# Optimization experiments

Measured on AMD Instinct MI355X. Metric: run time of the kernel, lower is better.

Reference implementation:

```python
import jax, jax.numpy as jnp
import numpy as np

B, S, H, NH = 16, 384, 1024, 16
HD = H // NH  # head_dim = 64

def setup_inputs() -> dict:
    key = jax.random.key(0)
    k1, k2, k3 = jax.random.split(key, 3)
    activation = jax.random.normal(k1, (B, S, H), dtype=jnp.float32)
    attention_mask = jnp.zeros((B, 1, 1, S), dtype=jnp.float32)  # additive mask
    qkv_weight = jax.random.normal(k2, (H, 3 * H), dtype=jnp.float32) * 0.02
    qkv_bias = jax.random.normal(k3, (3 * H,), dtype=jnp.float32) * 0.02
    return {"activation": activation, "attention_mask": attention_mask,
            "qkv_weight": qkv_weight, "qkv_bias": qkv_bias}

def reference(activation, attention_mask, qkv_weight, qkv_bias):
    # op1: fused QKV projection
    qkv = activation @ qkv_weight + qkv_bias            # [B,S,3H]
    q, k, v = jnp.split(qkv, 3, axis=-1)                # each [B,S,H]
    # op2-6: split heads -> [B,NH,S,HD]
    def heads(x):
        return x.reshape(B, S, NH, HD).transpose(0, 2, 1, 3)
    q, k, v = heads(q), heads(k), heads(v)
    # op7: QK^T
    scores = jnp.einsum('bhqd,bhkd->bhqk', q, k)        # [B,NH,S,S]
    # op8: scale + mask + softmax (scale applied to scores, then additive mask)
    scale = 1.0 / np.sqrt(HD).astype(np.float32)
    probs = jax.nn.softmax(scores * scale + attention_mask, axis=-1)
    # op9: weighted V
    out = jnp.einsum('bhqk,bhkd->bhqd', probs, v)       # [B,NH,S,HD]
    # op10: concat heads
    return out.transpose(0, 2, 1, 3).reshape(B, S, H)
```

## Files before the change

### kernel.cpp

```cpp
#include <hip/hip_runtime.h>
#include <hip/hip_bf16.h>

#define BB 16
#define SS 384
#define HH 1024
#define NH 16
#define HD 64
#define MM (BB*SS)
#define KK HH
#define N3 (3*HH)

typedef float f32x4 __attribute__((ext_vector_type(4)));
typedef __bf16 bf16x8 __attribute__((ext_vector_type(8)));
typedef unsigned short us8 __attribute__((ext_vector_type(8)));
typedef unsigned short us4 __attribute__((ext_vector_type(4)));

__device__ __forceinline__ void gload_lds16(const void* g, void* l) {
    __builtin_amdgcn_global_load_lds(
        (const __attribute__((address_space(1))) void*)g,
        (__attribute__((address_space(3))) void*)l, 16, 0, 0);
}

__device__ __forceinline__ unsigned short f2b(float f) {
    __bf16 h = (__bf16)f;
    return __builtin_bit_cast(unsigned short, h);
}

__global__ __launch_bounds__(256) void cvt_x(const float4* __restrict__ in,
                                             us4* __restrict__ out, int n4) {
    int i = blockIdx.x * 256 + threadIdx.x;
    if (i < n4) {
        float4 v = in[i];
        us4 o;
        o.x = f2b(v.x); o.y = f2b(v.y); o.z = f2b(v.z); o.w = f2b(v.w);
        out[i] = o;
    }
}

__global__ __launch_bounds__(256) void cvt_w(const float* __restrict__ Wf,
                                             __bf16* __restrict__ WT) {
    __shared__ float tile[32][33];
    const int n0 = blockIdx.x * 32, k0 = blockIdx.y * 32;
    const int t = threadIdx.x;
    const int tj = t & 31, ti = t >> 5;
#pragma unroll
    for (int p = 0; p < 4; ++p) {
        int i = p * 8 + ti;
        tile[i][tj] = Wf[(size_t)(k0 + i) * N3 + n0 + tj];
    }
    __syncthreads();
#pragma unroll
    for (int p = 0; p < 4; ++p) {
        int jj = p * 8 + ti;
        WT[(size_t)(n0 + jj) * KK + k0 + tj] = (__bf16)tile[tj][jj];
    }
}

__global__ __launch_bounds__(256) void qkv_gemm(const __bf16* __restrict__ Xb,
                                                const __bf16* __restrict__ WT,
                                                const float* __restrict__ bias,
                                                __bf16* __restrict__ QKb,
                                                __bf16* __restrict__ VTg) {
    __shared__ __bf16 As[128 * 32];
    __shared__ __bf16 Bs[128 * 32];
    const int t = threadIdx.x;
    const int w = t >> 6, lane = t & 63;
    const int wr = w >> 1, wc = w & 1;
    const int l15 = lane & 15, lg = lane >> 4;
    const int m0 = blockIdx.y * 128, n0 = blockIdx.x * 128;

    f32x4 acc[4][4] = {};

    for (int k0 = 0; k0 < KK; k0 += 32) {
#pragma unroll
        for (int i = 0; i < 2; ++i) {
            int slab = w * 2 + i;
            int row = slab * 16 + (lane >> 2);
            int ck = lane & 3;
            gload_lds16(Xb + (size_t)(m0 + row) * KK + k0 + ck * 8, &As[slab * 512]);
            gload_lds16(WT + (size_t)(n0 + row) * KK + k0 + ck * 8, &Bs[slab * 512]);
        }
        __syncthreads();

        bf16x8 a[4];
#pragma unroll
        for (int i = 0; i < 4; ++i) {
            int row = wr * 64 + i * 16 + l15;
            a[i] = *(const bf16x8*)&As[row * 32 + lg * 8];
        }
#pragma unroll
        for (int j = 0; j < 4; ++j) {
            int row = wc * 64 + j * 16 + l15;
            bf16x8 bv = *(const bf16x8*)&Bs[row * 32 + lg * 8];
#pragma unroll
            for (int i = 0; i < 4; ++i)
                acc[i][j] = __builtin_amdgcn_mfma_f32_16x16x32_bf16(a[i], bv, acc[i][j], 0, 0, 0);
        }
        __syncthreads();
    }

#pragma unroll
    for (int j = 0; j < 4; ++j) {
        int c = n0 + wc * 64 + j * 16 + l15;
        float bv = bias[c];
#pragma unroll
        for (int i = 0; i < 4; ++i) {
#pragma unroll
            for (int r = 0; r < 4; ++r) {
                int rr = m0 + wr * 64 + i * 16 + lg * 4 + r;
                float v = acc[i][j][r] + bv;
                if (c < 2048) {
                    QKb[(size_t)rr * 2048 + c] = (__bf16)v;
                } else {
                    int d = c & 63;
                    int hh = (c - 2048) >> 6;
                    int bb = rr / SS;
                    int s = rr - bb * SS;
                    VTg[((size_t)(bb * NH + hh) * HD + d) * SS + s] = (__bf16)v;
                }
            }
        }
    }
}

#define KLOFF 0
#define VTOFF 49152
#define PLOFF 98304
#define QLOFF 147456
#define MKOFF 155648
#define SMEMSZ 157184

__global__ __launch_bounds__(256) void attn(const __bf16* __restrict__ QKb,
                                            const __bf16* __restrict__ VTg,
                                            const float* __restrict__ maskg,
                                            float* __restrict__ out) {
    extern __shared__ char smem[];
    const int head = blockIdx.x;
    const int b = head >> 4, h = head & 15;
    const int t = threadIdx.x;
    const int w = t >> 6, lane = t & 63;
    const int l15 = lane & 15, lg = lane >> 4;

    for (int it = 0; it < 12; ++it) {
        int slot = it * 256 + t;
        int row = slot >> 3, ck = slot & 7;
        us8 v = *(const us8*)&QKb[(size_t)(b * SS + row) * 2048 + 1024 + h * 64 + ck * 8];
        int byte = (row * 128 + ck * 16) ^ ((row & 7) << 4);
        *(us8*)(smem + KLOFF + byte) = v;
    }
    for (int it = 0; it < 12; ++it) {
        int slot = it * 256 + t;
        int d = slot / 48, ck = slot - d * 48;
        us8 v = *(const us8*)&VTg[((size_t)head * HD + d) * SS + ck * 8];
        int byte = (d * 768 + ck * 16) ^ ((d & 7) << 4);
        *(us8*)(smem + VTOFF + byte) = v;
    }
    for (int s = t; s < SS; s += 256)
        ((float*)(smem + MKOFF))[s] = maskg[b * SS + s];
    __syncthreads();

    for (int q0 = 0; q0 < SS; q0 += 64) {
        for (int it = 0; it < 2; ++it) {
            int slot = it * 256 + t;
            int row = slot >> 3, ck = slot & 7;
            us8 v = *(const us8*)&QKb[(size_t)(b * SS + q0 + row) * 2048 + h * 64 + ck * 8];
            int byte = (row * 128 + ck * 16) ^ ((row & 7) << 4);
            *(us8*)(smem + QLOFF + byte) = v;
        }
        __syncthreads();

        f32x4 acc[24];
#pragma unroll
        for (int f = 0; f < 24; ++f) acc[f] = f32x4{0.f, 0.f, 0.f, 0.f};
        bf16x8 aq[2];
        {
            int row = w * 16 + l15;
#pragma unroll
            for (int st = 0; st < 2; ++st)
                aq[st] = *(const bf16x8*)(smem + QLOFF +
                          ((row * 128 + st * 64 + lg * 16) ^ ((row & 7) << 4)));
        }
#pragma unroll
        for (int f = 0; f < 24; ++f) {
            int row = f * 16 + l15;
#pragma unroll
            for (int st = 0; st < 2; ++st) {
                bf16x8 kb = *(const bf16x8*)(smem + KLOFF +
                             ((row * 128 + st * 64 + lg * 16) ^ ((row & 7) << 4)));
                acc[f] = __builtin_amdgcn_mfma_f32_16x16x32_bf16(aq[st], kb, acc[f], 0, 0, 0);
            }
        }

        const float* mrow = (const float*)(smem + MKOFF);
        float mx[4] = {-1e30f, -1e30f, -1e30f, -1e30f};
#pragma unroll
        for (int f = 0; f < 24; ++f) {
            float mk = mrow[f * 16 + l15];
#pragma unroll
            for (int r = 0; r < 4; ++r) {
                float v = acc[f][r] * 0.125f + mk;
                acc[f][r] = v;
                mx[r] = fmaxf(mx[r], v);
            }
        }
#pragma unroll
        for (int off = 8; off >= 1; off >>= 1)
#pragma unroll
            for (int r = 0; r < 4; ++r) mx[r] = fmaxf(mx[r], __shfl_xor(mx[r], off, 64));
        float sm[4] = {0.f, 0.f, 0.f, 0.f};
#pragma unroll
        for (int f = 0; f < 24; ++f)
#pragma unroll
            for (int r = 0; r < 4; ++r) {
                float p = __expf(acc[f][r] - mx[r]);
                acc[f][r] = p;
                sm[r] += p;
            }
#pragma unroll
        for (int off = 8; off >= 1; off >>= 1)
#pragma unroll
            for (int r = 0; r < 4; ++r) sm[r] += __shfl_xor(sm[r], off, 64);
        float inv[4];
#pragma unroll
        for (int r = 0; r < 4; ++r) inv[r] = 1.f / sm[r];

#pragma unroll
        for (int f = 0; f < 24; ++f)
#pragma unroll
            for (int r = 0; r < 4; ++r) {
                int row = w * 16 + lg * 4 + r;
                int col = f * 16 + l15;
                int byte = (row * 768 + col * 2) ^ ((row & 7) << 4);
                *(__bf16*)(smem + PLOFF + byte) = (__bf16)acc[f][r];
            }
        __syncthreads();

        f32x4 o[4] = {};
#pragma unroll
        for (int st = 0; st < 12; ++st) {
            int prow = w * 16 + l15;
            bf16x8 pa = *(const bf16x8*)(smem + PLOFF +
                         ((prow * 768 + st * 64 + lg * 16) ^ ((prow & 7) << 4)));
#pragma unroll
            for (int j = 0; j < 4; ++j) {
                int d = j * 16 + l15;
                bf16x8 vb = *(const bf16x8*)(smem + VTOFF +
                             ((d * 768 + st * 64 + lg * 16) ^ ((d & 7) << 4)));
                o[j] = __builtin_amdgcn_mfma_f32_16x16x32_bf16(pa, vb, o[j], 0, 0, 0);
            }
        }

#pragma unroll
        for (int j = 0; j < 4; ++j)
#pragma unroll
            for (int r = 0; r < 4; ++r) {
                int qrow = q0 + w * 16 + lg * 4 + r;
                out[(size_t)(b * SS + qrow) * HH + h * 64 + j * 16 + l15] =
                    o[j][r] * inv[r];
            }
    }
}

extern "C" void kernel_launch(void* const* d_in, const int* in_sizes, int n_in,
                              void* d_out, int out_size, void* d_ws, size_t ws_size,
                              hipStream_t stream) {
    const float* act  = (const float*)d_in[0];
    const float* mask = (const float*)d_in[1];
    const float* wq   = (const float*)d_in[2];
    const float* bias = (const float*)d_in[3];

    char* ws = (char*)d_ws;
    __bf16* Xb  = (__bf16*)(ws);
    __bf16* WT  = (__bf16*)(ws + 12582912);
    __bf16* QKb = (__bf16*)(ws + 18874368);
    __bf16* VTg = (__bf16*)(ws + 44040192);

    cvt_x<<<(MM * KK / 4 + 255) / 256, 256, 0, stream>>>((const float4*)act, (us4*)Xb, MM * KK / 4);
    cvt_w<<<dim3(N3 / 32, KK / 32), 256, 0, stream>>>(wq, WT);
    qkv_gemm<<<dim3(N3 / 128, MM / 128), 256, 0, stream>>>(Xb, WT, bias, QKb, VTg);

    (void)hipFuncSetAttribute((const void*)attn, hipFuncAttributeMaxDynamicSharedMemorySize, SMEMSZ);
    attn<<<BB * NH, 256, SMEMSZ, stream>>>(QKb, VTg, mask, (float*)d_out);
}
```

Before: 133.1 us.

## Double-buffer QKV GEMM LDS tiles, swizzle LDS chunks, remap blocks per XCD

The QKV GEMM main loop now double-buffers its LDS tiles, so the global-to-LDS load for the next K slice is issued before the MFMAs on the current slice, with one barrier per iteration. The 16-byte chunks within each LDS row are XOR-swizzled by row to cut bank conflicts on the fragment reads. The grid becomes a 1D launch of 1152 blocks, remapped so each of the 8 XCDs works on a contiguous 4x12 region of output tiles for better L2 locality. This doubles static LDS use per block, which may lower occupancy.

```diff
diff --git a/kernel.cpp b/kernel.cpp
--- a/kernel.cpp
+++ b/kernel.cpp
@@ -56,47 +56,70 @@
     }
 }
 
+__device__ __forceinline__ void stage_tile(const __bf16* __restrict__ A,
+                                           const __bf16* __restrict__ B,
+                                           __bf16* As, __bf16* Bs,
+                                           int w, int lane, int k0) {
+#pragma unroll
+    for (int i = 0; i < 2; ++i) {
+        int slab = w * 2 + i;
+        int row = slab * 16 + (lane >> 2);
+        int c   = lane & 3;
+        int cs  = c ^ ((row >> 1) & 3);
+        gload_lds16(A + (size_t)row * KK + k0 + cs * 8, As + slab * 512);
+        gload_lds16(B + (size_t)row * KK + k0 + cs * 8, Bs + slab * 512);
+    }
+}
+
 __global__ __launch_bounds__(256) void qkv_gemm(const __bf16* __restrict__ Xb,
                                                 const __bf16* __restrict__ WT,
                                                 const float* __restrict__ bias,
                                                 __bf16* __restrict__ QKb,
                                                 __bf16* __restrict__ VTg) {
-    __shared__ __bf16 As[128 * 32];
-    __shared__ __bf16 Bs[128 * 32];
+    __shared__ __bf16 As[2][128 * 32];
+    __shared__ __bf16 Bs[2][128 * 32];
     const int t = threadIdx.x;
     const int w = t >> 6, lane = t & 63;
     const int wr = w >> 1, wc = w & 1;
     const int l15 = lane & 15, lg = lane >> 4;
-    const int m0 = blockIdx.y * 128, n0 = blockIdx.x * 128;
+
+    const int bid = blockIdx.x;
+    const int xcd = bid & 7, loc = bid >> 3;
+    const int by = (xcd >> 1) * 12 + (loc / 12);
+    const int bx = (xcd & 1) * 12 + (loc % 12);
+    const int m0 = by * 128, n0 = bx * 128;
+
+    const __bf16* Ab = Xb + (size_t)m0 * KK;
+    const __bf16* Bb = WT + (size_t)n0 * KK;
 
     f32x4 acc[4][4] = {};
 
-    for (int k0 = 0; k0 < KK; k0 += 32) {
-#pragma unroll
-        for (int i = 0; i < 2; ++i) {
-            int slab = w * 2 + i;
-            int row = slab * 16 + (lane >> 2);
-            int ck = lane & 3;
-            gload_lds16(Xb + (size_t)(m0 + row) * KK + k0 + ck * 8, &As[slab * 512]);
-            gload_lds16(WT + (size_t)(n0 + row) * KK + k0 + ck * 8, &Bs[slab * 512]);
-        }
-        __syncthreads();
+    stage_tile(Ab, Bb, As[0], Bs[0], w, lane, 0);
+    __syncthreads();
+
+    int cur = 0;
+    for (int kt = 0; kt < 32; ++kt) {
+        if (kt + 1 < 32)
+            stage_tile(Ab, Bb, As[cur ^ 1], Bs[cur ^ 1], w, lane, (kt + 1) * 32);
 
         bf16x8 a[4];
 #pragma unroll
         for (int i = 0; i < 4; ++i) {
             int row = wr * 64 + i * 16 + l15;
-            a[i] = *(const bf16x8*)&As[row * 32 + lg * 8];
+            int ch = lg ^ ((row >> 1) & 3);
+            a[i] = *(const bf16x8*)&As[cur][row * 32 + ch * 8];
         }
 #pragma unroll
         for (int j = 0; j < 4; ++j) {
             int row = wc * 64 + j * 16 + l15;
-            bf16x8 bv = *(const bf16x8*)&Bs[row * 32 + lg * 8];
+            int ch = lg ^ ((row >> 1) & 3);
+            bf16x8 bv = *(const bf16x8*)&Bs[cur][row * 32 + ch * 8];
 #pragma unroll
             for (int i = 0; i < 4; ++i)
                 acc[i][j] = __builtin_amdgcn_mfma_f32_16x16x32_bf16(a[i], bv, acc[i][j], 0, 0, 0);
         }
         __syncthreads();
+        cur ^= 1;
     }
 
 #pragma unroll
@@ -277,7 +300,7 @@
 
     cvt_x<<<(MM * KK / 4 + 255) / 256, 256, 0, stream>>>((const float4*)act, (us4*)Xb, MM * KK / 4);
     cvt_w<<<dim3(N3 / 32, KK / 32), 256, 0, stream>>>(wq, WT);
-    qkv_gemm<<<dim3(N3 / 128, MM / 128), 256, 0, stream>>>(Xb, WT, bias, QKb, VTg);
+    qkv_gemm<<<dim3(1152), 256, 0, stream>>>(Xb, WT, bias, QKb, VTg);
 
     (void)hipFuncSetAttribute((const void*)attn, hipFuncAttributeMaxDynamicSharedMemorySize, SMEMSZ);
     attn<<<BB * NH, 256, SMEMSZ, stream>>>(QKb, VTg, mask, (float*)d_out);
```

After: 142.9 us. 7.4% more time.

## Triple-buffer QKV GEMM loads with swizzled LDS and XCD-aware block mapping

Applied to the files above, without the earlier changes.

Rewrites the QKV GEMM main loop as a three-stage software pipeline. Direct global-to-LDS loads for tiles two steps ahead are issued while the current tile is computed, with explicit vmcnt waits and one barrier per k-step. LDS columns are XOR-swizzled per row pair to reduce bank conflicts on the fragment reads. The 2D grid becomes a 1D grid remapped so each XCD gets a contiguous sub-block of output tiles, which should improve L2 reuse. The cost is triple the LDS footprint and hand-tuned waitcnt logic that must stay in step with the load count.

```diff
diff --git a/kernel.cpp b/kernel.cpp
--- a/kernel.cpp
+++ b/kernel.cpp
@@ -56,48 +56,80 @@
     }
 }
 
+#define KSTEP(KT, RB, SB, STG, VMC) do {                                      \
+    asm volatile("s_waitcnt vmcnt(" #VMC ")" ::: "memory");                   \
+    __builtin_amdgcn_s_barrier();                                             \
+    __builtin_amdgcn_sched_barrier(0);                                        \
+    if (STG) {                                                                \
+        const int ko = (KT + 2) * 32;                                         \
+        gload_lds16(Ap0 + ko, &As[SB][w * 1024]);                             \
+        gload_lds16(Ap1 + ko, &As[SB][w * 1024 + 512]);                       \
+        gload_lds16(Bp0 + ko, &Bs[SB][w * 1024]);                             \
+        gload_lds16(Bp1 + ko, &Bs[SB][w * 1024 + 512]);                       \
+    }                                                                         \
+    bf16x8 a[4];                                                              \
+    _Pragma("unroll")                                                         \
+    for (int i = 0; i < 4; ++i) {                                             \
+        int row = wr * 64 + i * 16 + l15;                                     \
+        int ch = lg ^ ((row >> 1) & 3);                                       \
+        a[i] = *(const bf16x8*)&As[RB][row * 32 + ch * 8];                    \
+    }                                                                         \
+    _Pragma("unroll")                                                         \
+    for (int j = 0; j < 4; ++j) {                                             \
+        int row = wc * 64 + j * 16 + l15;                                     \
+        int ch = lg ^ ((row >> 1) & 3);                                       \
+        bf16x8 bv = *(const bf16x8*)&Bs[RB][row * 32 + ch * 8];               \
+        _Pragma("unroll")                                                     \
+        for (int i = 0; i < 4; ++i)                                           \
+            acc[i][j] = __builtin_amdgcn_mfma_f32_16x16x32_bf16(a[i], bv, acc[i][j], 0, 0, 0); \
+    }                                                                         \
+} while (0)
+
 __global__ __launch_bounds__(256) void qkv_gemm(const __bf16* __restrict__ Xb,
                                                 const __bf16* __restrict__ WT,
                                                 const float* __restrict__ bias,
                                                 __bf16* __restrict__ QKb,
                                                 __bf16* __restrict__ VTg) {
-    __shared__ __bf16 As[128 * 32];
-    __shared__ __bf16 Bs[128 * 32];
+    __shared__ __bf16 As[3][128 * 32];
+    __shared__ __bf16 Bs[3][128 * 32];
     const int t = threadIdx.x;
     const int w = t >> 6, lane = t & 63;
     const int wr = w >> 1, wc = w & 1;
     const int l15 = lane & 15, lg = lane >> 4;
-    const int m0 = blockIdx.y * 128, n0 = blockIdx.x * 128;
+
+    const int bid = blockIdx.x;
+    const int xcd = bid & 7, loc = bid >> 3;
+    const int by = (xcd >> 1) * 12 + (loc / 12);
+    const int bx = (xcd & 1) * 12 + (loc % 12);
+    const int m0 = by * 128, n0 = bx * 128;
+
+    const int r0 = w * 32 + (lane >> 2);
+    const int r1 = r0 + 16;
+    const int c0 = (lane & 3) ^ ((r0 >> 1) & 3);
+    const int c1 = (lane & 3) ^ ((r1 >> 1) & 3);
+    const __bf16* Ap0 = Xb + (size_t)(m0 + r0) * KK + c0 * 8;
+    const __bf16* Ap1 = Xb + (size_t)(m0 + r1) * KK + c1 * 8;
+    const __bf16* Bp0 = WT + (size_t)(n0 + r0) * KK + c0 * 8;
+    const __bf16* Bp1 = WT + (size_t)(n0 + r1) * KK + c1 * 8;
 
     f32x4 acc[4][4] = {};
 
-    for (int k0 = 0; k0 < KK; k0 += 32) {
-#pragma unroll
-        for (int i = 0; i < 2; ++i) {
-            int slab = w * 2 + i;
-            int row = slab * 16 + (lane >> 2);
-            int ck = lane & 3;
-            gload_lds16(Xb + (size_t)(m0 + row) * KK + k0 + ck * 8, &As[slab * 512]);
-            gload_lds16(WT + (size_t)(n0 + row) * KK + k0 + ck * 8, &Bs[slab * 512]);
-        }
-        __syncthreads();
-
-        bf16x8 a[4];
-#pragma unroll
-        for (int i = 0; i < 4; ++i) {
-            int row = wr * 64 + i * 16 + l15;
-            a[i] = *(const bf16x8*)&As[row * 32 + lg * 8];
-        }
-#pragma unroll
-        for (int j = 0; j < 4; ++j) {
-            int row = wc * 64 + j * 16 + l15;
-            bf16x8 bv = *(const bf16x8*)&Bs[row * 32 + lg * 8];
-#pragma unroll
-            for (int i = 0; i < 4; ++i)
-                acc[i][j] = __builtin_amdgcn_mfma_f32_16x16x32_bf16(a[i], bv, acc[i][j], 0, 0, 0);
-        }
-        __syncthreads();
-    }
+    gload_lds16(Ap0 + 0,  &As[0][w * 1024]);
+    gload_lds16(Ap1 + 0,  &As[0][w * 1024 + 512]);
+    gload_lds16(Bp0 + 0,  &Bs[0][w * 1024]);
+    gload_lds16(Bp1 + 0,  &Bs[0][w * 1024 + 512]);
+    gload_lds16(Ap0 + 32, &As[1][w * 1024]);
+    gload_lds16(Ap1 + 32, &As[1][w * 1024 + 512]);
+    gload_lds16(Bp0 + 32, &Bs[1][w * 1024]);
+    gload_lds16(Bp1 + 32, &Bs[1][w * 1024 + 512]);
+
+    for (int g = 0; g < 30; g += 3) {
+        KSTEP(g + 0, 0, 2, 1, 4);
+        KSTEP(g + 1, 1, 0, 1, 4);
+        KSTEP(g + 2, 2, 1, 1, 4);
+    }
+    KSTEP(30, 0, 2, 0, 4);
+    KSTEP(31, 1, 0, 0, 0);
 
 #pragma unroll
     for (int j = 0; j < 4; ++j) {
@@ -277,7 +309,7 @@
 
     cvt_x<<<(MM * KK / 4 + 255) / 256, 256, 0, stream>>>((const float4*)act, (us4*)Xb, MM * KK / 4);
     cvt_w<<<dim3(N3 / 32, KK / 32), 256, 0, stream>>>(wq, WT);
-    qkv_gemm<<<dim3(N3 / 128, MM / 128), 256, 0, stream>>>(Xb, WT, bias, QKb, VTg);
+    qkv_gemm<<<dim3(1152), 256, 0, stream>>>(Xb, WT, bias, QKb, VTg);
 
     (void)hipFuncSetAttribute((const void*)attn, hipFuncAttributeMaxDynamicSharedMemorySize, SMEMSZ);
     attn<<<BB * NH, 256, SMEMSZ, stream>>>(QKb, VTg, mask, (float*)d_out);
```

Result: slower. 149.4 us (+12.3%).

## Split attention across query tiles per block, reading K/V directly from global

Applied to the files above, without the earlier changes.

The attention kernel now launches one block per (head, 64-row query tile), six times as many blocks, with an XCD-aware block-to-head mapping so tiles of the same head share an L2. K and V^T are no longer staged in LDS but read straight from global memory inside the MFMA loops. Only the probability tile uses shared memory, so LDS drops to 48KB and several blocks can fit per CU. This targets the low occupancy of the original 256-block launch, at the cost of repeated K/V global/L2 reads across the six query tiles.

```diff
diff --git a/kernel.cpp b/kernel.cpp
--- a/kernel.cpp
+++ b/kernel.cpp
@@ -123,142 +123,108 @@
     }
 }
 
-#define KLOFF 0
-#define VTOFF 49152
-#define PLOFF 98304
-#define QLOFF 147456
-#define MKOFF 155648
-#define SMEMSZ 157184
-
-__global__ __launch_bounds__(256) void attn(const __bf16* __restrict__ QKb,
-                                            const __bf16* __restrict__ VTg,
-                                            const float* __restrict__ maskg,
-                                            float* __restrict__ out) {
+#define SMEMSZ 49152
+
+__global__ __launch_bounds__(256, 3) void attn(const __bf16* __restrict__ QKb,
+                                               const __bf16* __restrict__ VTg,
+                                               const float* __restrict__ maskg,
+                                               float* __restrict__ out) {
     extern __shared__ char smem[];
-    const int head = blockIdx.x;
+    const int bid = blockIdx.x;
+    const int xcd = bid & 7, idx = bid >> 3;
+    const int head = xcd * 32 + idx / 6;
+    const int qt = idx - (idx / 6) * 6;
     const int b = head >> 4, h = head & 15;
+    const int q0 = qt * 64;
     const int t = threadIdx.x;
     const int w = t >> 6, lane = t & 63;
     const int l15 = lane & 15, lg = lane >> 4;
 
-    for (int it = 0; it < 12; ++it) {
-        int slot = it * 256 + t;
-        int row = slot >> 3, ck = slot & 7;
-        us8 v = *(const us8*)&QKb[(size_t)(b * SS + row) * 2048 + 1024 + h * 64 + ck * 8];
-        int byte = (row * 128 + ck * 16) ^ ((row & 7) << 4);
-        *(us8*)(smem + KLOFF + byte) = v;
-    }
-    for (int it = 0; it < 12; ++it) {
-        int slot = it * 256 + t;
-        int d = slot / 48, ck = slot - d * 48;
-        us8 v = *(const us8*)&VTg[((size_t)head * HD + d) * SS + ck * 8];
-        int byte = (d * 768 + ck * 16) ^ ((d & 7) << 4);
-        *(us8*)(smem + VTOFF + byte) = v;
-    }
-    for (int s = t; s < SS; s += 256)
-        ((float*)(smem + MKOFF))[s] = maskg[b * SS + s];
+    const size_t qrow = (size_t)(b * SS + q0 + w * 16 + l15) * 2048 + h * 64;
+    bf16x8 aq[2];
+#pragma unroll
+    for (int st = 0; st < 2; ++st)
+        aq[st] = *(const bf16x8*)&QKb[qrow + st * 32 + lg * 8];
+
+    f32x4 acc[24];
+#pragma unroll
+    for (int f = 0; f < 24; ++f) acc[f] = f32x4{0.f, 0.f, 0.f, 0.f};
+#pragma unroll
+    for (int f = 0; f < 24; ++f) {
+        const size_t krow = (size_t)(b * SS + f * 16 + l15) * 2048 + 1024 + h * 64;
+#pragma unroll
+        for (int st = 0; st < 2; ++st) {
+            bf16x8 kb = *(const bf16x8*)&QKb[krow + st * 32 + lg * 8];
+            acc[f] = __builtin_amdgcn_mfma_f32_16x16x32_bf16(aq[st], kb, acc[f], 0, 0, 0);
+        }
+    }
+
+    const float* mrow = maskg + b * SS;
+    float mx[4] = {-1e30f, -1e30f, -1e30f, -1e30f};
+#pragma unroll
+    for (int f = 0; f < 24; ++f) {
+        float mk = mrow[f * 16 + l15];
+#pragma unroll
+        for (int r = 0; r < 4; ++r) {
+            float v = acc[f][r] * 0.125f + mk;
+            acc[f][r] = v;
+            mx[r] = fmaxf(mx[r], v);
+        }
+    }
+#pragma unroll
+    for (int off = 8; off >= 1; off >>= 1)
+#pragma unroll
+        for (int r = 0; r < 4; ++r) mx[r] = fmaxf(mx[r], __shfl_xor(mx[r], off, 64));
+    float sm[4] = {0.f, 0.f, 0.f, 0.f};
+#pragma unroll
+    for (int f = 0; f < 24; ++f)
+#pragma unroll
+        for (int r = 0; r < 4; ++r) {
+            float p = __expf(acc[f][r] - mx[r]);
+            acc[f][r] = p;
+            sm[r] += p;
+        }
+#pragma unroll
+    for (int off = 8; off >= 1; off >>= 1)
+#pragma unroll
+        for (int r = 0; r < 4; ++r) sm[r] += __shfl_xor(sm[r], off, 64);
+    float inv[4];
+#pragma unroll
+    for (int r = 0; r < 4; ++r) inv[r] = 1.f / sm[r];
+
+#pragma unroll
+    for (int f = 0; f < 24; ++f)
+#pragma unroll
+        for (int r = 0; r < 4; ++r) {
+            int row = w * 16 + lg * 4 + r;
+            int col = f * 16 + l15;
+            int byte = (row * 768 + col * 2) ^ ((row & 7) << 4);
+            *(__bf16*)(smem + byte) = (__bf16)acc[f][r];
+        }
     __syncthreads();
 
-    for (int q0 = 0; q0 < SS; q0 += 64) {
-        for (int it = 0; it < 2; ++it) {
-            int slot = it * 256 + t;
-            int row = slot >> 3, ck = slot & 7;
-            us8 v = *(const us8*)&QKb[(size_t)(b * SS + q0 + row) * 2048 + h * 64 + ck * 8];
-            int byte = (row * 128 + ck * 16) ^ ((row & 7) << 4);
-            *(us8*)(smem + QLOFF + byte) = v;
-        }
-        __syncthreads();
-
-        f32x4 acc[24];
-#pragma unroll
-        for (int f = 0; f < 24; ++f) acc[f] = f32x4{0.f, 0.f, 0.f, 0.f};
-        bf16x8 aq[2];
-        {
-            int row = w * 16 + l15;
-#pragma unroll
-            for (int st = 0; st < 2; ++st)
-                aq[st] = *(const bf16x8*)(smem + QLOFF +
-                          ((row * 128 + st * 64 + lg * 16) ^ ((row & 7) << 4)));
-        }
-#pragma unroll
-        for (int f = 0; f < 24; ++f) {
-            int row = f * 16 + l15;
-#pragma unroll
-            for (int st = 0; st < 2; ++st) {
-                bf16x8 kb = *(const bf16x8*)(smem + KLOFF +
-                             ((row * 128 + st * 64 + lg * 16) ^ ((row & 7) << 4)));
-                acc[f] = __builtin_amdgcn_mfma_f32_16x16x32_bf16(aq[st], kb, acc[f], 0, 0, 0);
-            }
-        }
-
-        const float* mrow = (const float*)(smem + MKOFF);
-        float mx[4] = {-1e30f, -1e30f, -1e30f, -1e30f};
-#pragma unroll
-        for (int f = 0; f < 24; ++f) {
-            float mk = mrow[f * 16 + l15];
-#pragma unroll
-            for (int r = 0; r < 4; ++r) {
-                float v = acc[f][r] * 0.125f + mk;
-                acc[f][r] = v;
-                mx[r] = fmaxf(mx[r], v);
-            }
-        }
-#pragma unroll
-        for (int off = 8; off >= 1; off >>= 1)
-#pragma unroll
-            for (int r = 0; r < 4; ++r) mx[r] = fmaxf(mx[r], __shfl_xor(mx[r], off, 64));
-        float sm[4] = {0.f, 0.f, 0.f, 0.f};
-#pragma unroll
-        for (int f = 0; f < 24; ++f)
-#pragma unroll
-            for (int r = 0; r < 4; ++r) {
-                float p = __expf(acc[f][r] - mx[r]);
-                acc[f][r] = p;
-                sm[r] += p;
-            }
-#pragma unroll
-        for (int off = 8; off >= 1; off >>= 1)
-#pragma unroll
-            for (int r = 0; r < 4; ++r) sm[r] += __shfl_xor(sm[r], off, 64);
-        float inv[4];
-#pragma unroll
-        for (int r = 0; r < 4; ++r) inv[r] = 1.f / sm[r];
-
-#pragma unroll
-        for (int f = 0; f < 24; ++f)
-#pragma unroll
-            for (int r = 0; r < 4; ++r) {
-                int row = w * 16 + lg * 4 + r;
-                int col = f * 16 + l15;
-                int byte = (row * 768 + col * 2) ^ ((row & 7) << 4);
-                *(__bf16*)(smem + PLOFF + byte) = (__bf16)acc[f][r];
-            }
-        __syncthreads();
-
-        f32x4 o[4] = {};
-#pragma unroll
-        for (int st = 0; st < 12; ++st) {
-            int prow = w * 16 + l15;
-            bf16x8 pa = *(const bf16x8*)(smem + PLOFF +
-                         ((prow * 768 + st * 64 + lg * 16) ^ ((prow & 7) << 4)));
-#pragma unroll
-            for (int j = 0; j < 4; ++j) {
-                int d = j * 16 + l15;
-                bf16x8 vb = *(const bf16x8*)(smem + VTOFF +
-                             ((d * 768 + st * 64 + lg * 16) ^ ((d & 7) << 4)));
-                o[j] = __builtin_amdgcn_mfma_f32_16x16x32_bf16(pa, vb, o[j], 0, 0, 0);
-            }
-        }
-
-#pragma unroll
-        for (int j = 0; j < 4; ++j)
-#pragma unroll
-            for (int r = 0; r < 4; ++r) {
-                int qrow = q0 + w * 16 + lg * 4 + r;
-                out[(size_t)(b * SS + qrow) * HH + h * 64 + j * 16 + l15] =
-                    o[j][r] * inv[r];
-            }
-    }
+    f32x4 o[4] = {};
+    const int prow = w * 16 + l15;
+#pragma unroll
+    for (int st = 0; st < 12; ++st) {
+        bf16x8 pa = *(const bf16x8*)(smem +
+                     ((prow * 768 + st * 64 + lg * 16) ^ ((prow & 7) << 4)));
+#pragma unroll
+        for (int j = 0; j < 4; ++j) {
+            bf16x8 vb = *(const bf16x8*)&VTg[((size_t)head * HD + j * 16 + l15) * SS
+                                             + st * 32 + lg * 8];
+            o[j] = __builtin_amdgcn_mfma_f32_16x16x32_bf16(pa, vb, o[j], 0, 0, 0);
+        }
+    }
+
+#pragma unroll
+    for (int j = 0; j < 4; ++j)
+#pragma unroll
+        for (int r = 0; r < 4; ++r) {
+            int qr = q0 + w * 16 + lg * 4 + r;
+            out[(size_t)(b * SS + qr) * HH + h * 64 + j * 16 + l15] =
+                o[j][r] * inv[r];
+        }
 }
 
 extern "C" void kernel_launch(void* const* d_in, const int* in_sizes, int n_in,
@@ -280,5 +246,5 @@
     qkv_gemm<<<dim3(N3 / 128, MM / 128), 256, 0, stream>>>(Xb, WT, bias, QKb, VTg);
 
     (void)hipFuncSetAttribute((const void*)attn, hipFuncAttributeMaxDynamicSharedMemorySize, SMEMSZ);
-    attn<<<BB * NH, 256, SMEMSZ, stream>>>(QKb, VTg, mask, (float*)d_out);
-}
+    attn<<<BB * NH * 6, 256, SMEMSZ, stream>>>(QKb, VTg, mask, (float*)d_out);
+}
```

New measurement: 165.4 us. 1.24x slower.
